# Kernel tuning notes

Hardware: AMD Instinct MI355X
Metric: run time of the kernel (lower is better)

The kernel has to match this reference:

```python
import jax, jax.numpy as jnp
import numpy as np

N = 50000       # nodes
E = 1600000     # edges (avg degree 32)
DIM = 256       # args.dim (input feature dim)
OUT = 64        # args.n_classes (output dim)
ALPHA = 0.2     # leaky relu negative slope


def setup_inputs() -> dict:
    key = jax.random.key(0)
    k1, k2, k3, k4 = jax.random.split(key, 4)
    x = jax.random.normal(k1, (N, DIM), dtype=jnp.float32)
    # sparse adjacency as COO indices: row 0 = src (output row), row 1 = dst (neighbor)
    edge_index = jax.random.randint(k2, (2, E), 0, N, dtype=jnp.int32)
    # xavier-uniform init as in SpGraphAttentionLayer
    lim_w = float(np.sqrt(6.0 / (DIM + OUT)))
    W = jax.random.uniform(k3, (DIM, OUT), minval=-lim_w, maxval=lim_w, dtype=jnp.float32)
    lim_a = float(np.sqrt(6.0 / (1 + 2 * OUT)))
    a = jax.random.uniform(k4, (2 * OUT,), minval=-lim_a, maxval=lim_a, dtype=jnp.float32)
    return {"x": x, "edge_index": edge_index, "W": W, "a": a}


def reference(x, edge_index, W, a):
    # h = x @ W : [N, OUT]
    h = x @ W
    src = edge_index[0]  # [E] output row index i
    dst = edge_index[1]  # [E] neighbor index j
    # attention logit per edge: a . concat(h[i], h[j])
    logits = h[src] @ a[:OUT] + h[dst] @ a[OUT:]          # [E]
    # edge_e = exp(-leakyrelu(logits))  (note the negation, as in SpGraphAttentionLayer)
    e = jnp.exp(-jax.nn.leaky_relu(logits, ALPHA))         # [E]
    # row-wise normalizer: sum_j e_ij
    rowsum = jax.ops.segment_sum(e, src, num_segments=N)   # [N]
    # aggregated messages: sum_j e_ij * h_j
    agg = jax.ops.segment_sum(e[:, None] * h[dst], src, num_segments=N)  # [N, OUT]
    # h' = agg / rowsum, then elu (concat=True branch)
    return jax.nn.elu(agg / rowsum[:, None])
```

## Files before the change

kernel.cpp:

```cpp
#include <hip/hip_runtime.h>

#define NN 50000
#define NE 1600000
#define DIM 256
#define OUTD 64
#define ALPHA 0.2f

#define BSH 6
#define NB ((NN + 63) >> 6)
#define CAP 3072
#define P1 128
#define EPB (NE / P1)

#define GEMM_BLOCKS ((NN + 63) / 64)
#define WSTRIDE 264

typedef unsigned short u16;
typedef unsigned int u32;
typedef __attribute__((ext_vector_type(8))) short short8;
typedef __attribute__((ext_vector_type(4))) float floatx4;

__device__ __forceinline__ u16 f2bf(float f) {
  u32 b = __float_as_uint(f);
  b += 0x7FFFu + ((b >> 16) & 1u);
  return (u16)(b >> 16);
}
__device__ __forceinline__ float bflo(u32 u) { return __uint_as_float(u << 16); }
__device__ __forceinline__ float bfhi(u32 u) { return __uint_as_float(u & 0xFFFF0000u); }

__global__ __launch_bounds__(256) void init_kernel(const float* __restrict__ W,
                                                   u32* __restrict__ wt,
                                                   int* __restrict__ bktcnt) {
  if (blockIdx.x < 4) {
    const int i = blockIdx.x * 256 + threadIdx.x;
    if (i < NB) bktcnt[i] = 0;
    return;
  }
  const int g = (blockIdx.x - 4) * 256 + threadIdx.x;
  const int n = g >> 7;
  const int kp = g & 127;
  const float lo = W[(size_t)(2 * kp) * OUTD + n];
  const float hi = W[(size_t)(2 * kp + 1) * OUTD + n];
  wt[g] = (u32)f2bf(lo) | ((u32)f2bf(hi) << 16);
}

__global__ __launch_bounds__(256) void gemm_kernel(
    const float* __restrict__ x, const u32* __restrict__ wt,
    const float* __restrict__ a, u16* __restrict__ hb,
    float* __restrict__ s1, float* __restrict__ s2)
{
  __shared__ u16 Wl[OUTD * WSTRIDE];
  const int t = threadIdx.x;
  {
    const uint4* srcv = (const uint4*)wt;
#pragma unroll
    for (int i = 0; i < 8; ++i) {
      const int c = t + 256 * i;
      const int n = c >> 5;
      const int k8 = c & 31;
      *(uint4*)&Wl[n * WSTRIDE + k8 * 8] = srcv[c];
    }
  }
  __syncthreads();

  const int lane = t & 63;
  const int wv = t >> 6;
  const int n = lane & 15;
  const int quad = lane >> 4;
  int rb = blockIdx.x * 64 + wv * 16;
  if (rb > NN - 16) rb = NN - 16;
  const int row = rb + n;
  const float4* xrow = (const float4*)(x + (size_t)row * DIM);

  floatx4 acc[4] = {{0.f, 0.f, 0.f, 0.f},
                    {0.f, 0.f, 0.f, 0.f},
                    {0.f, 0.f, 0.f, 0.f},
                    {0.f, 0.f, 0.f, 0.f}};

#pragma unroll
  for (int kk = 0; kk < 8; ++kk) {
    const float4 lo = xrow[kk * 8 + quad * 2];
    const float4 hi = xrow[kk * 8 + quad * 2 + 1];
    union { u32 u[4]; short8 s; } af;
    af.u[0] = (u32)f2bf(lo.x) | ((u32)f2bf(lo.y) << 16);
    af.u[1] = (u32)f2bf(lo.z) | ((u32)f2bf(lo.w) << 16);
    af.u[2] = (u32)f2bf(hi.x) | ((u32)f2bf(hi.y) << 16);
    af.u[3] = (u32)f2bf(hi.z) | ((u32)f2bf(hi.w) << 16);
#pragma unroll
    for (int nt = 0; nt < 4; ++nt) {
      const short8 bf =
          *(const short8*)&Wl[(nt * 16 + n) * WSTRIDE + kk * 32 + quad * 8];
      acc[nt] = __builtin_amdgcn_mfma_f32_16x16x32_bf16(af.s, bf, acc[nt], 0, 0, 0);
    }
  }

  float av1[4], av2[4];
#pragma unroll
  for (int nt = 0; nt < 4; ++nt) {
    av1[nt] = a[nt * 16 + n];
    av2[nt] = a[OUTD + nt * 16 + n];
  }

#pragma unroll
  for (int reg = 0; reg < 4; ++reg) {
    const int r = rb + quad * 4 + reg;
    float q1 = acc[0][reg] * av1[0] + acc[1][reg] * av1[1] +
               acc[2][reg] * av1[2] + acc[3][reg] * av1[3];
    float q2 = acc[0][reg] * av2[0] + acc[1][reg] * av2[1] +
               acc[2][reg] * av2[2] + acc[3][reg] * av2[3];
#pragma unroll
    for (int off = 1; off <= 8; off <<= 1) {
      q1 += __shfl_xor(q1, off);
      q2 += __shfl_xor(q2, off);
    }
    if (n == 0) { s1[r] = q1; s2[r] = q2; }
#pragma unroll
    for (int nt = 0; nt < 4; ++nt)
      hb[(size_t)r * OUTD + nt * 16 + n] = f2bf(acc[nt][reg]);
  }
}

__global__ __launch_bounds__(1024) void bin_kernel(
    const int* __restrict__ src, const int* __restrict__ dst,
    int* __restrict__ bktcnt, u32* __restrict__ binned)
{
  __shared__ int lh[NB];
  const int t = threadIdx.x;
  const int p = blockIdx.x;
  for (int i = t; i < NB; i += 1024) lh[i] = 0;
  __syncthreads();

  const int4* src4 = (const int4*)(src + p * EPB);
  const int4* dst4 = (const int4*)(dst + p * EPB);
  for (int i = t; i < EPB / 4; i += 1024) {
    const int4 s = src4[i];
    if ((u32)s.x < (u32)NN) atomicAdd(&lh[s.x >> BSH], 1);
    if ((u32)s.y < (u32)NN) atomicAdd(&lh[s.y >> BSH], 1);
    if ((u32)s.z < (u32)NN) atomicAdd(&lh[s.z >> BSH], 1);
    if ((u32)s.w < (u32)NN) atomicAdd(&lh[s.w >> BSH], 1);
  }
  __syncthreads();

  for (int b = t; b < NB; b += 1024) {
    const int c = lh[b];
    lh[b] = (c > 0) ? atomicAdd(bktcnt + b, c) + b * CAP : 0;
  }
  __syncthreads();

  for (int i = t; i < EPB / 4; i += 1024) {
    const int4 s = src4[i];
    const int4 d = dst4[i];
    int pos, b;
    if ((u32)s.x < (u32)NN) {
      b = s.x >> BSH; pos = atomicAdd(&lh[b], 1);
      if (pos < (b + 1) * CAP) binned[pos] = ((u32)(s.x & 63) << 16) | (u32)(d.x & 0xFFFF);
    }
    if ((u32)s.y < (u32)NN) {
      b = s.y >> BSH; pos = atomicAdd(&lh[b], 1);
      if (pos < (b + 1) * CAP) binned[pos] = ((u32)(s.y & 63) << 16) | (u32)(d.y & 0xFFFF);
    }
    if ((u32)s.z < (u32)NN) {
      b = s.z >> BSH; pos = atomicAdd(&lh[b], 1);
      if (pos < (b + 1) * CAP) binned[pos] = ((u32)(s.z & 63) << 16) | (u32)(d.z & 0xFFFF);
    }
    if ((u32)s.w < (u32)NN) {
      b = s.w >> BSH; pos = atomicAdd(&lh[b], 1);
      if (pos < (b + 1) * CAP) binned[pos] = ((u32)(s.w & 63) << 16) | (u32)(d.w & 0xFFFF);
    }
  }
}

__global__ __launch_bounds__(256) void group_kernel(
    const u32* __restrict__ binned, const int* __restrict__ bktcnt,
    int* __restrict__ rowstart, int* __restrict__ deg,
    u16* __restrict__ edst16)
{
  __shared__ int cnt[64];
  __shared__ int off[64];
  const int b = blockIdx.x;
  const int t = threadIdx.x;
  int n = bktcnt[b];
  if (n > CAP) n = CAP;
  if (t < 64) cnt[t] = 0;
  __syncthreads();

  const u32* eb = binned + (size_t)b * CAP;
  for (int i = t; i < n; i += 256)
    atomicAdd(&cnt[(eb[i] >> 16) & 63], 1);
  __syncthreads();

  if (t < 64) {
    const int v = cnt[t];
    int xx = v;
#pragma unroll
    for (int o = 1; o < 64; o <<= 1) {
      const int y = __shfl_up(xx, o, 64);
      if (t >= o) xx += y;
    }
    off[t] = xx - v;
    const int node = b * 64 + t;
    if (node < NN) {
      rowstart[node] = b * CAP + xx - v;
      deg[node] = v;
    }
  }
  __syncthreads();

  for (int i = t; i < n; i += 256) {
    const u32 pv = eb[i];
    const int pos = atomicAdd(&off[(pv >> 16) & 63], 1);
    edst16[(size_t)b * CAP + pos] = (u16)(pv & 0xFFFFu);
  }
}

__global__ __launch_bounds__(256) void agg_kernel(
    const u16* __restrict__ hb, const float* __restrict__ s1,
    const float* __restrict__ s2, const int* __restrict__ pre,
    const int* __restrict__ deg, const u16* __restrict__ edst,
    float* __restrict__ out)
{
  const int lane = threadIdx.x & 63;
  const int g = lane >> 3;
  const int seg = lane & 7;
  const int node =
      __builtin_amdgcn_readfirstlane(blockIdx.x * 4 + (threadIdx.x >> 6));
  const int base = pre[node];
  const int cnt = deg[node];
  const float s1i = s1[node];

  float a0 = 0.f, a1 = 0.f, a2 = 0.f, a3 = 0.f;
  float a4 = 0.f, a5 = 0.f, a6 = 0.f, a7 = 0.f;
  float wsum = 0.f;

  for (int c0 = 0; c0 < cnt; c0 += 64) {
    const int m = min(64, cnt - c0);
    int d = 0;
    float w = 0.f;
    if (lane < m) {
      d = edst[(size_t)base + c0 + lane];
      const float logit = s1i + s2[d];
      const float lr = logit > 0.f ? logit : ALPHA * logit;
      w = __expf(-lr);
    }
#pragma unroll 4
    for (int e = 0; e < m; e += 8) {
      const int idx = e + g;
      const int dg = __shfl(d, idx);
      const float wg = __shfl(w, idx);
      const uint4 p = *(const uint4*)(hb + (size_t)dg * OUTD + seg * 8);
      a0 = fmaf(wg, bflo(p.x), a0);
      a1 = fmaf(wg, bfhi(p.x), a1);
      a2 = fmaf(wg, bflo(p.y), a2);
      a3 = fmaf(wg, bfhi(p.y), a3);
      a4 = fmaf(wg, bflo(p.z), a4);
      a5 = fmaf(wg, bfhi(p.z), a5);
      a6 = fmaf(wg, bflo(p.w), a6);
      a7 = fmaf(wg, bfhi(p.w), a7);
      wsum += wg;
    }
  }

#pragma unroll
  for (int off = 8; off <= 32; off <<= 1) {
    a0 += __shfl_xor(a0, off);
    a1 += __shfl_xor(a1, off);
    a2 += __shfl_xor(a2, off);
    a3 += __shfl_xor(a3, off);
    a4 += __shfl_xor(a4, off);
    a5 += __shfl_xor(a5, off);
    a6 += __shfl_xor(a6, off);
    a7 += __shfl_xor(a7, off);
    wsum += __shfl_xor(wsum, off);
  }

  if (g == 0) {
    const float inv = (cnt > 0) ? 1.f / wsum : 0.f;
    float4 r;
    float v;
    v = a0 * inv; r.x = v > 0.f ? v : (__expf(v) - 1.f);
    v = a1 * inv; r.y = v > 0.f ? v : (__expf(v) - 1.f);
    v = a2 * inv; r.z = v > 0.f ? v : (__expf(v) - 1.f);
    v = a3 * inv; r.w = v > 0.f ? v : (__expf(v) - 1.f);
    *(float4*)(out + (size_t)node * OUTD + seg * 8) = r;
    v = a4 * inv; r.x = v > 0.f ? v : (__expf(v) - 1.f);
    v = a5 * inv; r.y = v > 0.f ? v : (__expf(v) - 1.f);
    v = a6 * inv; r.z = v > 0.f ? v : (__expf(v) - 1.f);
    v = a7 * inv; r.w = v > 0.f ? v : (__expf(v) - 1.f);
    *(float4*)(out + (size_t)node * OUTD + seg * 8 + 4) = r;
  }
}

extern "C" void kernel_launch(void* const* d_in, const int* in_sizes, int n_in,
                              void* d_out, int out_size, void* d_ws, size_t ws_size,
                              hipStream_t stream) {
  const float* x = (const float*)d_in[0];
  const int* ei = (const int*)d_in[1];
  const float* W = (const float*)d_in[2];
  const float* a = (const float*)d_in[3];
  float* out = (float*)d_out;

  u16* hb = (u16*)d_ws;
  float* s1 = (float*)(hb + (size_t)NN * OUTD);
  float* s2 = s1 + NN;
  int* rowstart = (int*)(s2 + NN);
  int* deg = rowstart + NN;
  int* bktcnt = deg + NN;
  u32* wt = (u32*)(bktcnt + NB);
  u32* binned = wt + 8192;
  u16* edst16 = (u16*)(binned + (size_t)NB * CAP);

  const int* src = ei;
  const int* dst = ei + NE;

  hipLaunchKernelGGL(init_kernel, dim3(36), dim3(256), 0, stream, W, wt, bktcnt);
  hipLaunchKernelGGL(gemm_kernel, dim3(GEMM_BLOCKS), dim3(256), 0, stream,
                     x, wt, a, hb, s1, s2);
  hipLaunchKernelGGL(bin_kernel, dim3(P1), dim3(1024), 0, stream,
                     src, dst, bktcnt, binned);
  hipLaunchKernelGGL(group_kernel, dim3(NB), dim3(256), 0, stream,
                     binned, bktcnt, rowstart, deg, edst16);
  hipLaunchKernelGGL(agg_kernel, dim3(NN / 4), dim3(256), 0, stream,
                     hb, s1, s2, rowstart, deg, edst16, out);
}
```

Baseline: 168.3 us.

## Fuse bucket grouping and aggregation into one LDS-resident kernel per bucket

Merges the group and agg kernels into a single per-bucket kernel. Each block loads its bucket's edges into shared memory, counting-sorts them by local node, and computes the edge weights once into LDS. Eight waves then aggregate eight nodes each by reading neighbor indices and weights from LDS. This drops the global edst16, rowstart and deg round-trip and one launch. The cost is about 30KB of LDS per block, only 782 blocks of 512 threads, and serial per-node loops within a wave, which may reduce occupancy and parallelism.

```diff
diff --git a/kernel.cpp b/kernel.cpp
--- a/kernel.cpp
+++ b/kernel.cpp
@@ -170,23 +170,36 @@
   }
 }
 
-__global__ __launch_bounds__(256) void group_kernel(
-    const u32* __restrict__ binned, const int* __restrict__ bktcnt,
-    int* __restrict__ rowstart, int* __restrict__ deg,
-    u16* __restrict__ edst16)
+__global__ __launch_bounds__(512) void bucket_agg_kernel(
+    const u16* __restrict__ hb, const float* __restrict__ s1,
+    const float* __restrict__ s2, const int* __restrict__ bktcnt,
+    const u32* __restrict__ binned, float* __restrict__ out)
 {
+  __shared__ u32 ebuf[CAP];
+  __shared__ u16 sdst[CAP];
+  __shared__ float wls[CAP];
+  __shared__ float s1l[64];
   __shared__ int cnt[64];
-  __shared__ int off[64];
+  __shared__ int off0[64];
+  __shared__ int cur[64];
   const int b = blockIdx.x;
   const int t = threadIdx.x;
   int n = bktcnt[b];
   if (n > CAP) n = CAP;
-  if (t < 64) cnt[t] = 0;
+
+  if (t < 64) {
+    cnt[t] = 0;
+    const int nd = b * 64 + t;
+    s1l[t] = (nd < NN) ? s1[nd] : 0.f;
+  }
   __syncthreads();
 
   const u32* eb = binned + (size_t)b * CAP;
-  for (int i = t; i < n; i += 256)
-    atomicAdd(&cnt[(eb[i] >> 16) & 63], 1);
+  for (int i = t; i < n; i += 512) {
+    const u32 v = eb[i];
+    ebuf[i] = v;
+    atomicAdd(&cnt[(v >> 16) & 63], 1);
+  }
   __syncthreads();
 
   if (t < 64) {
@@ -197,56 +210,42 @@
       const int y = __shfl_up(xx, o, 64);
       if (t >= o) xx += y;
     }
-    off[t] = xx - v;
-    const int node = b * 64 + t;
-    if (node < NN) {
-      rowstart[node] = b * CAP + xx - v;
-      deg[node] = v;
-    }
-  }
-  __syncthreads();
-
-  for (int i = t; i < n; i += 256) {
-    const u32 pv = eb[i];
-    const int pos = atomicAdd(&off[(pv >> 16) & 63], 1);
-    edst16[(size_t)b * CAP + pos] = (u16)(pv & 0xFFFFu);
-  }
-}
-
-__global__ __launch_bounds__(256) void agg_kernel(
-    const u16* __restrict__ hb, const float* __restrict__ s1,
-    const float* __restrict__ s2, const int* __restrict__ pre,
-    const int* __restrict__ deg, const u16* __restrict__ edst,
-    float* __restrict__ out)
-{
-  const int lane = threadIdx.x & 63;
+    off0[t] = xx - v;
+    cur[t] = xx - v;
+  }
+  __syncthreads();
+
+  for (int i = t; i < n; i += 512) {
+    const u32 v = ebuf[i];
+    const int ln = (v >> 16) & 63;
+    const int d = (int)(v & 0xFFFFu);
+    const int pos = atomicAdd(&cur[ln], 1);
+    sdst[pos] = (u16)d;
+    const float logit = s1l[ln] + s2[d];
+    const float lr = logit > 0.f ? logit : ALPHA * logit;
+    wls[pos] = __expf(-lr);
+  }
+  __syncthreads();
+
+  const int lane = t & 63;
+  const int wv = t >> 6;
   const int g = lane >> 3;
   const int seg = lane & 7;
-  const int node =
-      __builtin_amdgcn_readfirstlane(blockIdx.x * 4 + (threadIdx.x >> 6));
-  const int base = pre[node];
-  const int cnt = deg[node];
-  const float s1i = s1[node];
-
-  float a0 = 0.f, a1 = 0.f, a2 = 0.f, a3 = 0.f;
-  float a4 = 0.f, a5 = 0.f, a6 = 0.f, a7 = 0.f;
-  float wsum = 0.f;
-
-  for (int c0 = 0; c0 < cnt; c0 += 64) {
-    const int m = min(64, cnt - c0);
-    int d = 0;
-    float w = 0.f;
-    if (lane < m) {
-      d = edst[(size_t)base + c0 + lane];
-      const float logit = s1i + s2[d];
-      const float lr = logit > 0.f ? logit : ALPHA * logit;
-      w = __expf(-lr);
-    }
-#pragma unroll 4
-    for (int e = 0; e < m; e += 8) {
-      const int idx = e + g;
-      const int dg = __shfl(d, idx);
-      const float wg = __shfl(w, idx);
+
+  for (int ni = 0; ni < 8; ++ni) {
+    const int ln = wv * 8 + ni;
+    const int node = b * 64 + ln;
+    if (node >= NN) continue;
+    const int base = off0[ln];
+    const int cend = base + cnt[ln];
+
+    float a0 = 0.f, a1 = 0.f, a2 = 0.f, a3 = 0.f;
+    float a4 = 0.f, a5 = 0.f, a6 = 0.f, a7 = 0.f;
+    float wsum = 0.f;
+
+    for (int e = base + g; e < cend; e += 8) {
+      const int dg = sdst[e];
+      const float wg = wls[e];
       const uint4 p = *(const uint4*)(hb + (size_t)dg * OUTD + seg * 8);
       a0 = fmaf(wg, bflo(p.x), a0);
       a1 = fmaf(wg, bfhi(p.x), a1);
@@ -258,35 +257,35 @@
       a7 = fmaf(wg, bfhi(p.w), a7);
       wsum += wg;
     }
-  }
-
-#pragma unroll
-  for (int off = 8; off <= 32; off <<= 1) {
-    a0 += __shfl_xor(a0, off);
-    a1 += __shfl_xor(a1, off);
-    a2 += __shfl_xor(a2, off);
-    a3 += __shfl_xor(a3, off);
-    a4 += __shfl_xor(a4, off);
-    a5 += __shfl_xor(a5, off);
-    a6 += __shfl_xor(a6, off);
-    a7 += __shfl_xor(a7, off);
-    wsum += __shfl_xor(wsum, off);
-  }
-
-  if (g == 0) {
-    const float inv = (cnt > 0) ? 1.f / wsum : 0.f;
-    float4 r;
-    float v;
-    v = a0 * inv; r.x = v > 0.f ? v : (__expf(v) - 1.f);
-    v = a1 * inv; r.y = v > 0.f ? v : (__expf(v) - 1.f);
-    v = a2 * inv; r.z = v > 0.f ? v : (__expf(v) - 1.f);
-    v = a3 * inv; r.w = v > 0.f ? v : (__expf(v) - 1.f);
-    *(float4*)(out + (size_t)node * OUTD + seg * 8) = r;
-    v = a4 * inv; r.x = v > 0.f ? v : (__expf(v) - 1.f);
-    v = a5 * inv; r.y = v > 0.f ? v : (__expf(v) - 1.f);
-    v = a6 * inv; r.z = v > 0.f ? v : (__expf(v) - 1.f);
-    v = a7 * inv; r.w = v > 0.f ? v : (__expf(v) - 1.f);
-    *(float4*)(out + (size_t)node * OUTD + seg * 8 + 4) = r;
+
+#pragma unroll
+    for (int off = 8; off <= 32; off <<= 1) {
+      a0 += __shfl_xor(a0, off);
+      a1 += __shfl_xor(a1, off);
+      a2 += __shfl_xor(a2, off);
+      a3 += __shfl_xor(a3, off);
+      a4 += __shfl_xor(a4, off);
+      a5 += __shfl_xor(a5, off);
+      a6 += __shfl_xor(a6, off);
+      a7 += __shfl_xor(a7, off);
+      wsum += __shfl_xor(wsum, off);
+    }
+
+    if (g == 0) {
+      const float inv = (cnt[ln] > 0) ? 1.f / wsum : 0.f;
+      float4 r;
+      float v;
+      v = a0 * inv; r.x = v > 0.f ? v : (__expf(v) - 1.f);
+      v = a1 * inv; r.y = v > 0.f ? v : (__expf(v) - 1.f);
+      v = a2 * inv; r.z = v > 0.f ? v : (__expf(v) - 1.f);
+      v = a3 * inv; r.w = v > 0.f ? v : (__expf(v) - 1.f);
+      *(float4*)(out + (size_t)node * OUTD + seg * 8) = r;
+      v = a4 * inv; r.x = v > 0.f ? v : (__expf(v) - 1.f);
+      v = a5 * inv; r.y = v > 0.f ? v : (__expf(v) - 1.f);
+      v = a6 * inv; r.z = v > 0.f ? v : (__expf(v) - 1.f);
+      v = a7 * inv; r.w = v > 0.f ? v : (__expf(v) - 1.f);
+      *(float4*)(out + (size_t)node * OUTD + seg * 8 + 4) = r;
+    }
   }
 }
 
@@ -302,12 +301,9 @@
   u16* hb = (u16*)d_ws;
   float* s1 = (float*)(hb + (size_t)NN * OUTD);
   float* s2 = s1 + NN;
-  int* rowstart = (int*)(s2 + NN);
-  int* deg = rowstart + NN;
-  int* bktcnt = deg + NN;
+  int* bktcnt = (int*)(s2 + NN);
   u32* wt = (u32*)(bktcnt + NB);
   u32* binned = wt + 8192;
-  u16* edst16 = (u16*)(binned + (size_t)NB * CAP);
 
   const int* src = ei;
   const int* dst = ei + NE;
@@ -317,8 +313,6 @@
                      x, wt, a, hb, s1, s2);
   hipLaunchKernelGGL(bin_kernel, dim3(P1), dim3(1024), 0, stream,
                      src, dst, bktcnt, binned);
-  hipLaunchKernelGGL(group_kernel, dim3(NB), dim3(256), 0, stream,
-                     binned, bktcnt, rowstart, deg, edst16);
-  hipLaunchKernelGGL(agg_kernel, dim3(NN / 4), dim3(256), 0, stream,
-                     hb, s1, s2, rowstart, deg, edst16, out);
-}
+  hipLaunchKernelGGL(bucket_agg_kernel, dim3(NB), dim3(512), 0, stream,
+                     hb, s1, s2, bktcnt, binned, out);
+}
```

Measured after the change: 163.2 us. -3.0%, faster.
